# Optimization experiments

Measured on AMD Instinct MI355X. Metric: run time of the kernel, lower is better.

The kernel has to match this reference:

```python
import jax, jax.numpy as jnp
import numpy as np

WINDOW_SIZE = 11
SIGMA = 1.5
C1 = 0.01 ** 2
C2 = 0.03 ** 2


def _gaussian_window(channel, dtype):
    # 1D gaussian, normalized, then outer product -> 2D window, expanded per channel
    xs = np.arange(WINDOW_SIZE) - WINDOW_SIZE // 2
    g = np.exp(-(xs.astype(np.float64) ** 2) / (2.0 * SIGMA ** 2))
    g = (g / g.sum()).astype(np.float32)
    w2d = np.outer(g, g)  # [ws, ws]
    w = np.broadcast_to(w2d[None, None], (channel, 1, WINDOW_SIZE, WINDOW_SIZE))
    return jnp.asarray(w, dtype=dtype)


def _depthwise_conv(img, window, channel):
    pad = WINDOW_SIZE // 2
    return jax.lax.conv_general_dilated(
        img, window,
        window_strides=(1, 1),
        padding=[(pad, pad), (pad, pad)],
        dimension_numbers=('NCHW', 'OIHW', 'NCHW'),
        feature_group_count=channel)


def setup_inputs() -> dict:
    key = jax.random.key(0)
    k1, k2 = jax.random.split(key)
    shape = (16, 3, 512, 512)
    x = jax.random.uniform(k1, shape, dtype=jnp.float32)
    y = jax.random.uniform(k2, shape, dtype=jnp.float32)
    return {"x": x, "y": y}


def reference(x, y):
    channel = x.shape[-3]
    window = _gaussian_window(channel, x.dtype)

    mu1 = _depthwise_conv(x, window, channel)
    mu2 = _depthwise_conv(y, window, channel)
    mu1_sq = mu1 * mu1
    mu2_sq = mu2 * mu2
    mu1_mu2 = mu1 * mu2
    sigma1_sq = _depthwise_conv(x * x, window, channel) - mu1_sq
    sigma2_sq = _depthwise_conv(y * y, window, channel) - mu2_sq
    sigma12 = _depthwise_conv(x * y, window, channel) - mu1_mu2

    ssim_map = ((2.0 * mu1_mu2 + C1) * (2.0 * sigma12 + C2)) / (
        (mu1_sq + mu2_sq + C1) * (sigma1_sq + sigma2_sq + C2))
    # DSSIM = 1 - mean(ssim)
    return 1.0 - jnp.mean(ssim_map)
```

## Files before the change

### kernel.cpp

```cpp
#include <hip/hip_runtime.h>


typedef _Float16 half8 __attribute__((ext_vector_type(8)));
typedef _Float16 half4v __attribute__((ext_vector_type(4)));
typedef float f32x4 __attribute__((ext_vector_type(4)));
typedef float f32x8 __attribute__((ext_vector_type(8)));

#define IMG_W   512
#define IMG_H   512
#define NPLANES 48
#define BR      16
#define TP      40
#define GRX     (IMG_H / BR)
#define NBLK    (GRX * NPLANES)

__global__ __launch_bounds__(256, 3)
void dssim_main(const float* __restrict__ xin, const float* __restrict__ yin,
                float* __restrict__ partial) {
    __shared__ _Float16 ldsT[4][2][4][16][TP];
    __shared__ float wpart[4];

    const int t    = threadIdx.x;
    const int lane = t & 63;
    const int wid  = t >> 6;
    const int bn   = lane & 15;
    const int jg   = lane >> 4;
    const int r0   = blockIdx.x * BR;
    const size_t pbase = (size_t)blockIdx.y * (IMG_W * IMG_H);
    const float* __restrict__ xp = xin + pbase;
    const float* __restrict__ yp = yin + pbase;

    float ginv;
    {
        float s = 0.f;
#pragma unroll
        for (int i = 0; i < 11; ++i) {
            float d = (float)(i - 5);
            s += expf(-(d * d) * (1.0f / 4.5f));
        }
        ginv = 1.0f / s;
    }

    half8 whF, wvF;
#pragma unroll
    for (int j = 0; j < 8; ++j) {
        const int k = 8 * jg + j;
        const int dh = k - bn - 3;
        const int dv = k - bn;
        float wh = 0.f, wv = 0.f;
        if (dh >= 0 && dh < 11) {
            const float d = (float)(dh - 5);
            wh = ginv * expf(-(d * d) * (1.0f / 4.5f));
        }
        if (dv >= 0 && dv < 11) {
            const float d = (float)(dv - 5);
            wv = ginv * expf(-(d * d) * (1.0f / 4.5f));
        }
        whF[j] = (_Float16)wh;
        wvF[j] = (_Float16)wv;
    }

    const int gr0 = r0 - 5 + bn;
    const bool rowok0 = (gr0 >= 0) && (gr0 < IMG_H);
    const int gr1 = r0 + 11 + bn;
    const bool rowok1 = (bn < 10) && (gr1 < IMG_H);
    const size_t row0 = (size_t)(rowok0 ? gr0 : 0) * IMG_W;
    const size_t row1 = (size_t)(rowok1 ? gr1 : 0) * IMG_W;

    const f32x8 z8 = {0.f, 0.f, 0.f, 0.f, 0.f, 0.f, 0.f, 0.f};
    const f32x4 zf = {0.f, 0.f, 0.f, 0.f};
    const float C1 = 0.0001f, C2 = 0.0009f;
    float lsum = 0.f;

    f32x8 xs0, ys0, xs1, ys1;

#define LOADI(ii)                                                           \
    {                                                                       \
        const int col = (((wid + 4 * (ii)) << 4) + 8 * jg) - 8;             \
        const bool colok = (col >= 0) && (col < IMG_W);                     \
        const size_t co = (size_t)(colok ? col : 0);                        \
        const bool ok0 = colok && rowok0, ok1 = colok && rowok1;            \
        xs0 = ok0 ? *(const f32x8*)(xp + row0 + co) : z8;                   \
        ys0 = ok0 ? *(const f32x8*)(yp + row0 + co) : z8;                   \
        xs1 = ok1 ? *(const f32x8*)(xp + row1 + co) : z8;                   \
        ys1 = ok1 ? *(const f32x8*)(yp + row1 + co) : z8;                   \
    }

#define HCOMPI(ii)                                                          \
    {                                                                       \
        const int slot = (ii) & 1;                                          \
        _Pragma("unroll")                                                   \
        for (int rt = 0; rt < 2; ++rt) {                                    \
            const f32x8 xv = rt ? xs1 : xs0;                                \
            const f32x8 yv = rt ? ys1 : ys0;                                \
            half8 aU, aW, aU2, aW2;                                         \
            _Pragma("unroll")                                               \
            for (int d = 0; d < 8; ++d) {                                   \
                aU[d] = (_Float16)(xv[d] + yv[d]);                          \
                aW[d] = (_Float16)(xv[d] - yv[d]);                          \
            }                                                               \
            _Pragma("unroll")                                               \
            for (int d = 0; d < 8; ++d) {                                   \
                aU2[d] = aU[d] * aU[d];                                     \
                aW2[d] = aW[d] * aW[d];                                     \
            }                                                               \
            const f32x4 cU  = __builtin_amdgcn_mfma_f32_16x16x32_f16(aU,  whF, zf, 0, 0, 0); \
            const f32x4 cW  = __builtin_amdgcn_mfma_f32_16x16x32_f16(aW,  whF, zf, 0, 0, 0); \
            const f32x4 cU2 = __builtin_amdgcn_mfma_f32_16x16x32_f16(aU2, whF, zf, 0, 0, 0); \
            const f32x4 cW2 = __builtin_amdgcn_mfma_f32_16x16x32_f16(aW2, whF, zf, 0, 0, 0); \
            half4v hU, hW, hU2, hW2;                                        \
            _Pragma("unroll")                                               \
            for (int q = 0; q < 4; ++q) {                                   \
                hU[q]  = (_Float16)cU[q];                                   \
                hW[q]  = (_Float16)cW[q];                                   \
                hU2[q] = (_Float16)cU2[q];                                  \
                hW2[q] = (_Float16)cW2[q];                                  \
            }                                                               \
            const int kk = 16 * rt + 4 * jg;                                \
            *(half4v*)&ldsT[wid][slot][0][bn][kk] = hU;                     \
            *(half4v*)&ldsT[wid][slot][1][bn][kk] = hW;                     \
            *(half4v*)&ldsT[wid][slot][2][bn][kk] = hU2;                    \
            *(half4v*)&ldsT[wid][slot][3][bn][kk] = hW2;                    \
        }                                                                   \
    }

#define VBLURI(ii)                                                          \
    {                                                                       \
        const int slot = (ii) & 1;                                          \
        const half8 aTU  = *(const half8*)&ldsT[wid][slot][0][bn][8 * jg];  \
        const half8 aTW  = *(const half8*)&ldsT[wid][slot][1][bn][8 * jg];  \
        const half8 aTU2 = *(const half8*)&ldsT[wid][slot][2][bn][8 * jg];  \
        const half8 aTW2 = *(const half8*)&ldsT[wid][slot][3][bn][8 * jg];  \
        const f32x4 accU = __builtin_amdgcn_mfma_f32_16x16x32_f16(aTU,  wvF, zf, 0, 0, 0); \
        const f32x4 accW = __builtin_amdgcn_mfma_f32_16x16x32_f16(aTW,  wvF, zf, 0, 0, 0); \
        const f32x4 accP = __builtin_amdgcn_mfma_f32_16x16x32_f16(aTU2, wvF, zf, 0, 0, 0); \
        const f32x4 accQ = __builtin_amdgcn_mfma_f32_16x16x32_f16(aTW2, wvF, zf, 0, 0, 0); \
        _Pragma("unroll")                                                   \
        for (int q = 0; q < 4; ++q) {                                       \
            const float U = accU[q], W = accW[q];                           \
            const float P = accP[q], Q = accQ[q];                           \
            const float U2 = U * U, W2 = W * W;                             \
            const float A = 0.5f * (U2 + W2);                               \
            const float B = 0.5f * (U2 - W2);                               \
            const float den2 = fmaf(0.5f, P + Q, -A) + C2;                  \
            const float num2 = fmaf(0.5f, P - Q, -B) + C2;                  \
            lsum += (B + C1) * num2 * __builtin_amdgcn_rcpf((A + C1) * den2); \
        }                                                                   \
    }

    LOADI(0);
    HCOMPI(0);
#pragma unroll
    for (int i = 0; i < 8; ++i) {
        if (i + 1 < 8) LOADI(i + 1);
        VBLURI(i);
        if (i + 1 < 8) HCOMPI(i + 1);
    }

#pragma unroll
    for (int off = 32; off >= 1; off >>= 1)
        lsum += __shfl_down(lsum, off, 64);
    if (lane == 0) wpart[wid] = lsum;
    __syncthreads();
    if (t == 0) {
        partial[(size_t)blockIdx.y * GRX + blockIdx.x] =
            wpart[0] + wpart[1] + wpart[2] + wpart[3];
    }
}

__global__ __launch_bounds__(256)
void dssim_final(const float* __restrict__ partial, float* __restrict__ out) {
    __shared__ double wsum[4];
    double s = 0.0;
    for (int i = threadIdx.x; i < NBLK; i += 256) s += (double)partial[i];
#pragma unroll
    for (int off = 32; off >= 1; off >>= 1)
        s += __shfl_down(s, off, 64);
    if ((threadIdx.x & 63) == 0) wsum[threadIdx.x >> 6] = s;
    __syncthreads();
    if (threadIdx.x == 0) {
        const double tot = wsum[0] + wsum[1] + wsum[2] + wsum[3];
        out[0] = (float)(1.0 - tot / 12582912.0);
    }
}

extern "C" void kernel_launch(void* const* d_in, const int* in_sizes, int n_in,
                              void* d_out, int out_size, void* d_ws, size_t ws_size,
                              hipStream_t stream) {
    const float* x = (const float*)d_in[0];
    const float* y = (const float*)d_in[1];
    float* out = (float*)d_out;
    float* partial = (float*)d_ws;

    dim3 grid(GRX, NPLANES);
    dim3 block(256);
    dssim_main<<<grid, block, 0, stream>>>(x, y, partial);
    dssim_final<<<1, block, 0, stream>>>(partial, out);
}
```

Before: 49.01 us.

## Single-buffer LDS transpose with XOR swizzle, packed fp16 converts, higher occupancy

The per-wave LDS transpose buffer goes from double to single buffering, which halves shared memory per block. The launch bound is raised from 3 to 5 blocks per CU to use that headroom. An XOR swizzle on the column index is meant to cut LDS bank conflicts, and the scalar fp16 conversions become packed cvt_pkrtz (round toward zero) with vector half multiplies. With only one buffer there is a write-after-read hazard between iterations, unless ordering within the wave covers it. The rounding mode also changes from nearest to toward-zero.

After: 113.3 us. 2.31x slower.

```diff
diff --git a/kernel.cpp b/kernel.cpp
--- a/kernel.cpp
+++ b/kernel.cpp
@@ -3,6 +3,7 @@
 
 typedef _Float16 half8 __attribute__((ext_vector_type(8)));
 typedef _Float16 half4v __attribute__((ext_vector_type(4)));
+typedef __fp16 pk16 __attribute__((ext_vector_type(2)));
 typedef float f32x4 __attribute__((ext_vector_type(4)));
 typedef float f32x8 __attribute__((ext_vector_type(8)));
 
@@ -14,10 +15,10 @@
 #define GRX     (IMG_H / BR)
 #define NBLK    (GRX * NPLANES)
 
-__global__ __launch_bounds__(256, 3)
+__global__ __launch_bounds__(256, 5)
 void dssim_main(const float* __restrict__ xin, const float* __restrict__ yin,
                 float* __restrict__ partial) {
-    __shared__ _Float16 ldsT[4][2][4][16][TP];
+    __shared__ _Float16 ldsT[4][4][16][TP];
     __shared__ float wpart[4];
 
     const int t    = threadIdx.x;
@@ -25,6 +26,7 @@
     const int wid  = t >> 6;
     const int bn   = lane & 15;
     const int jg   = lane >> 4;
+    const int swz  = (bn & 8) << 1;
     const int r0   = blockIdx.x * BR;
     const size_t pbase = (size_t)blockIdx.y * (IMG_W * IMG_H);
     const float* __restrict__ xp = xin + pbase;
@@ -88,49 +90,53 @@
 
 #define HCOMPI(ii)                                                          \
     {                                                                       \
-        const int slot = (ii) & 1;                                          \
         _Pragma("unroll")                                                   \
         for (int rt = 0; rt < 2; ++rt) {                                    \
             const f32x8 xv = rt ? xs1 : xs0;                                \
             const f32x8 yv = rt ? ys1 : ys0;                                \
-            half8 aU, aW, aU2, aW2;                                         \
+            half8 aU, aW;                                                   \
             _Pragma("unroll")                                               \
-            for (int d = 0; d < 8; ++d) {                                   \
-                aU[d] = (_Float16)(xv[d] + yv[d]);                          \
-                aW[d] = (_Float16)(xv[d] - yv[d]);                          \
+            for (int d = 0; d < 4; ++d) {                                   \
+                const pk16 pu = __builtin_amdgcn_cvt_pkrtz(                 \
+                    xv[2 * d] + yv[2 * d], xv[2 * d + 1] + yv[2 * d + 1]);  \
+                const pk16 pw = __builtin_amdgcn_cvt_pkrtz(                 \
+                    xv[2 * d] - yv[2 * d], xv[2 * d + 1] - yv[2 * d + 1]);  \
+                aU[2 * d] = (_Float16)pu[0]; aU[2 * d + 1] = (_Float16)pu[1]; \
+                aW[2 * d] = (_Float16)pw[0]; aW[2 * d + 1] = (_Float16)pw[1]; \
             }                                                               \
-            _Pragma("unroll")                                               \
-            for (int d = 0; d < 8; ++d) {                                   \
-                aU2[d] = aU[d] * aU[d];                                     \
-                aW2[d] = aW[d] * aW[d];                                     \
-            }                                                               \
+            const half8 aU2 = aU * aU;                                      \
+            const half8 aW2 = aW * aW;                                      \
             const f32x4 cU  = __builtin_amdgcn_mfma_f32_16x16x32_f16(aU,  whF, zf, 0, 0, 0); \
             const f32x4 cW  = __builtin_amdgcn_mfma_f32_16x16x32_f16(aW,  whF, zf, 0, 0, 0); \
             const f32x4 cU2 = __builtin_amdgcn_mfma_f32_16x16x32_f16(aU2, whF, zf, 0, 0, 0); \
             const f32x4 cW2 = __builtin_amdgcn_mfma_f32_16x16x32_f16(aW2, whF, zf, 0, 0, 0); \
             half4v hU, hW, hU2, hW2;                                        \
             _Pragma("unroll")                                               \
-            for (int q = 0; q < 4; ++q) {                                   \
-                hU[q]  = (_Float16)cU[q];                                   \
-                hW[q]  = (_Float16)cW[q];                                   \
-                hU2[q] = (_Float16)cU2[q];                                  \
-                hW2[q] = (_Float16)cW2[q];                                  \
+            for (int q = 0; q < 2; ++q) {                                   \
+                const pk16 p0 = __builtin_amdgcn_cvt_pkrtz(cU[2*q],  cU[2*q+1]);  \
+                const pk16 p1 = __builtin_amdgcn_cvt_pkrtz(cW[2*q],  cW[2*q+1]);  \
+                const pk16 p2 = __builtin_amdgcn_cvt_pkrtz(cU2[2*q], cU2[2*q+1]); \
+                const pk16 p3 = __builtin_amdgcn_cvt_pkrtz(cW2[2*q], cW2[2*q+1]); \
+                hU[2*q]  = (_Float16)p0[0]; hU[2*q+1]  = (_Float16)p0[1];   \
+                hW[2*q]  = (_Float16)p1[0]; hW[2*q+1]  = (_Float16)p1[1];   \
+                hU2[2*q] = (_Float16)p2[0]; hU2[2*q+1] = (_Float16)p2[1];   \
+                hW2[2*q] = (_Float16)p3[0]; hW2[2*q+1] = (_Float16)p3[1];   \
             }                                                               \
-            const int kk = 16 * rt + 4 * jg;                                \
-            *(half4v*)&ldsT[wid][slot][0][bn][kk] = hU;                     \
-            *(half4v*)&ldsT[wid][slot][1][bn][kk] = hW;                     \
-            *(half4v*)&ldsT[wid][slot][2][bn][kk] = hU2;                    \
-            *(half4v*)&ldsT[wid][slot][3][bn][kk] = hW2;                    \
+            const int kk = (16 * rt + 4 * jg) ^ swz;                        \
+            *(half4v*)&ldsT[wid][0][bn][kk] = hU;                           \
+            *(half4v*)&ldsT[wid][1][bn][kk] = hW;                           \
+            *(half4v*)&ldsT[wid][2][bn][kk] = hU2;                          \
+            *(half4v*)&ldsT[wid][3][bn][kk] = hW2;                          \
         }                                                                   \
     }
 
 #define VBLURI(ii)                                                          \
     {                                                                       \
-        const int slot = (ii) & 1;                                          \
-        const half8 aTU  = *(const half8*)&ldsT[wid][slot][0][bn][8 * jg];  \
-        const half8 aTW  = *(const half8*)&ldsT[wid][slot][1][bn][8 * jg];  \
-        const half8 aTU2 = *(const half8*)&ldsT[wid][slot][2][bn][8 * jg];  \
-        const half8 aTW2 = *(const half8*)&ldsT[wid][slot][3][bn][8 * jg];  \
+        const int kb = (8 * jg) ^ swz;                                      \
+        const half8 aTU  = *(const half8*)&ldsT[wid][0][bn][kb];            \
+        const half8 aTW  = *(const half8*)&ldsT[wid][1][bn][kb];            \
+        const half8 aTU2 = *(const half8*)&ldsT[wid][2][bn][kb];            \
+        const half8 aTW2 = *(const half8*)&ldsT[wid][3][bn][kb];            \
         const f32x4 accU = __builtin_amdgcn_mfma_f32_16x16x32_f16(aTU,  wvF, zf, 0, 0, 0); \
         const f32x4 accW = __builtin_amdgcn_mfma_f32_16x16x32_f16(aTW,  wvF, zf, 0, 0, 0); \
         const f32x4 accP = __builtin_amdgcn_mfma_f32_16x16x32_f16(aTU2, wvF, zf, 0, 0, 0); \
```

## Keep horizontal-blur MFMA results in registers, dropping the LDS transpose

Applied to the files above, without the earlier changes.

The horizontal-pass MFMA outputs are now packed straight into register operands for the vertical pass. The operands are swapped so the output layout of the first MFMA matches the B-operand layout of the second, with the vertical weights re-indexed to suit, so the LDS store, reload and shared buffer are gone. Column bounds checks are replaced by fixed pointer offsets that clamp only the two edge lanes, and row checks now run only for edge blocks. Conversions use packed round-toward-zero f16 conversion, which changes rounding slightly and adds some risk of subtle indexing errors.

Result: slower. 53.49 us (+9.2%).

```diff
diff --git a/kernel.cpp b/kernel.cpp
--- a/kernel.cpp
+++ b/kernel.cpp
@@ -2,7 +2,7 @@
 
 
 typedef _Float16 half8 __attribute__((ext_vector_type(8)));
-typedef _Float16 half4v __attribute__((ext_vector_type(4)));
+typedef __fp16 pk16 __attribute__((ext_vector_type(2)));
 typedef float f32x4 __attribute__((ext_vector_type(4)));
 typedef float f32x8 __attribute__((ext_vector_type(8)));
 
@@ -10,14 +10,12 @@
 #define IMG_H   512
 #define NPLANES 48
 #define BR      16
-#define TP      40
 #define GRX     (IMG_H / BR)
 #define NBLK    (GRX * NPLANES)
 
 __global__ __launch_bounds__(256, 3)
 void dssim_main(const float* __restrict__ xin, const float* __restrict__ yin,
                 float* __restrict__ partial) {
-    __shared__ _Float16 ldsT[4][2][4][16][TP];
     __shared__ float wpart[4];
 
     const int t    = threadIdx.x;
@@ -26,6 +24,7 @@
     const int bn   = lane & 15;
     const int jg   = lane >> 4;
     const int r0   = blockIdx.x * BR;
+    const bool edge = (blockIdx.x == 0) || (blockIdx.x == GRX - 1);
     const size_t pbase = (size_t)blockIdx.y * (IMG_W * IMG_H);
     const float* __restrict__ xp = xin + pbase;
     const float* __restrict__ yp = yin + pbase;
@@ -46,7 +45,8 @@
     for (int j = 0; j < 8; ++j) {
         const int k = 8 * jg + j;
         const int dh = k - bn - 3;
-        const int dv = k - bn;
+        const int sigma = (j < 4) ? (4 * jg + j) : (12 + 4 * jg + j);
+        const int dv = sigma - bn;
         float wh = 0.f, wv = 0.f;
         if (dh >= 0 && dh < 11) {
             const float d = (float)(dh - 5);
@@ -67,74 +67,99 @@
     const size_t row0 = (size_t)(rowok0 ? gr0 : 0) * IMG_W;
     const size_t row1 = (size_t)(rowok1 ? gr1 : 0) * IMG_W;
 
+    const int cb = (wid << 4) + (jg << 3) - 8;
+    const float* bx0 = xp + row0 + cb;
+    const float* by0 = yp + row0 + cb;
+    const float* bx1 = xp + row1 + cb;
+    const float* by1 = yp + row1 + cb;
+
     const f32x8 z8 = {0.f, 0.f, 0.f, 0.f, 0.f, 0.f, 0.f, 0.f};
     const f32x4 zf = {0.f, 0.f, 0.f, 0.f};
     const float C1 = 0.0001f, C2 = 0.0009f;
     float lsum = 0.f;
 
     f32x8 xs0, ys0, xs1, ys1;
-
-#define LOADI(ii)                                                           \
+    half8 bU, bW, bP, bQ;
+
+#define LOADP(m)                                                            \
     {                                                                       \
-        const int col = (((wid + 4 * (ii)) << 4) + 8 * jg) - 8;             \
-        const bool colok = (col >= 0) && (col < IMG_W);                     \
-        const size_t co = (size_t)(colok ? col : 0);                        \
-        const bool ok0 = colok && rowok0, ok1 = colok && rowok1;            \
-        xs0 = ok0 ? *(const f32x8*)(xp + row0 + co) : z8;                   \
-        ys0 = ok0 ? *(const f32x8*)(yp + row0 + co) : z8;                   \
-        xs1 = ok1 ? *(const f32x8*)(xp + row1 + co) : z8;                   \
-        ys1 = ok1 ? *(const f32x8*)(yp + row1 + co) : z8;                   \
-    }
-
-#define HCOMPI(ii)                                                          \
+        int fix = 0;                                                        \
+        if ((m) == 0) fix = (wid == 0 && jg == 0) ? 8 : 0;                  \
+        if ((m) == 7) fix = (wid == 3 && jg == 3) ? -8 : 0;                 \
+        const int off = 64 * (m);                                           \
+        xs0 = *(const f32x8*)(bx0 + off + fix);                             \
+        ys0 = *(const f32x8*)(by0 + off + fix);                             \
+        xs1 = *(const f32x8*)(bx1 + off + fix);                             \
+        ys1 = *(const f32x8*)(by1 + off + fix);                             \
+        if ((m) == 0) {                                                     \
+            if (wid == 0 && jg == 0) { xs0 = z8; ys0 = z8; xs1 = z8; ys1 = z8; } \
+        }                                                                   \
+        if ((m) == 7) {                                                     \
+            if (wid == 3 && jg == 3) { xs0 = z8; ys0 = z8; xs1 = z8; ys1 = z8; } \
+        }                                                                   \
+        if (edge) {                                                         \
+            if (!rowok0) { xs0 = z8; ys0 = z8; }                            \
+            if (!rowok1) { xs1 = z8; ys1 = z8; }                            \
+        }                                                                   \
+    }
+
+#define HCOMP()                                                             \
     {                                                                       \
-        const int slot = (ii) & 1;                                          \
+        half8 aU0, aW0, aU1, aW1;                                           \
         _Pragma("unroll")                                                   \
-        for (int rt = 0; rt < 2; ++rt) {                                    \
-            const f32x8 xv = rt ? xs1 : xs0;                                \
-            const f32x8 yv = rt ? ys1 : ys0;                                \
-            half8 aU, aW, aU2, aW2;                                         \
-            _Pragma("unroll")                                               \
-            for (int d = 0; d < 8; ++d) {                                   \
-                aU[d] = (_Float16)(xv[d] + yv[d]);                          \
-                aW[d] = (_Float16)(xv[d] - yv[d]);                          \
-            }                                                               \
-            _Pragma("unroll")                                               \
-            for (int d = 0; d < 8; ++d) {                                   \
-                aU2[d] = aU[d] * aU[d];                                     \
-                aW2[d] = aW[d] * aW[d];                                     \
-            }                                                               \
-            const f32x4 cU  = __builtin_amdgcn_mfma_f32_16x16x32_f16(aU,  whF, zf, 0, 0, 0); \
-            const f32x4 cW  = __builtin_amdgcn_mfma_f32_16x16x32_f16(aW,  whF, zf, 0, 0, 0); \
-            const f32x4 cU2 = __builtin_amdgcn_mfma_f32_16x16x32_f16(aU2, whF, zf, 0, 0, 0); \
-            const f32x4 cW2 = __builtin_amdgcn_mfma_f32_16x16x32_f16(aW2, whF, zf, 0, 0, 0); \
-            half4v hU, hW, hU2, hW2;                                        \
-            _Pragma("unroll")                                               \
-            for (int q = 0; q < 4; ++q) {                                   \
-                hU[q]  = (_Float16)cU[q];                                   \
-                hW[q]  = (_Float16)cW[q];                                   \
-                hU2[q] = (_Float16)cU2[q];                                  \
-                hW2[q] = (_Float16)cW2[q];                                  \
-            }                                                               \
-            const int kk = 16 * rt + 4 * jg;                                \
-            *(half4v*)&ldsT[wid][slot][0][bn][kk] = hU;                     \
-            *(half4v*)&ldsT[wid][slot][1][bn][kk] = hW;                     \
-            *(half4v*)&ldsT[wid][slot][2][bn][kk] = hU2;                    \
-            *(half4v*)&ldsT[wid][slot][3][bn][kk] = hW2;                    \
-        }                                                                   \
-    }
-
-#define VBLURI(ii)                                                          \
+        for (int d = 0; d < 4; ++d) {                                       \
+            const pk16 pu0 = __builtin_amdgcn_cvt_pkrtz(                    \
+                xs0[2 * d] + ys0[2 * d], xs0[2 * d + 1] + ys0[2 * d + 1]);  \
+            const pk16 pw0 = __builtin_amdgcn_cvt_pkrtz(                    \
+                xs0[2 * d] - ys0[2 * d], xs0[2 * d + 1] - ys0[2 * d + 1]);  \
+            const pk16 pu1 = __builtin_amdgcn_cvt_pkrtz(                    \
+                xs1[2 * d] + ys1[2 * d], xs1[2 * d + 1] + ys1[2 * d + 1]);  \
+            const pk16 pw1 = __builtin_amdgcn_cvt_pkrtz(                    \
+                xs1[2 * d] - ys1[2 * d], xs1[2 * d + 1] - ys1[2 * d + 1]);  \
+            aU0[2 * d] = (_Float16)pu0[0]; aU0[2 * d + 1] = (_Float16)pu0[1]; \
+            aW0[2 * d] = (_Float16)pw0[0]; aW0[2 * d + 1] = (_Float16)pw0[1]; \
+            aU1[2 * d] = (_Float16)pu1[0]; aU1[2 * d + 1] = (_Float16)pu1[1]; \
+            aW1[2 * d] = (_Float16)pw1[0]; aW1[2 * d + 1] = (_Float16)pw1[1]; \
+        }                                                                   \
+        const half8 aP0 = aU0 * aU0;                                        \
+        const half8 aQ0 = aW0 * aW0;                                        \
+        const half8 aP1 = aU1 * aU1;                                        \
+        const half8 aQ1 = aW1 * aW1;                                        \
+        const f32x4 cU0 = __builtin_amdgcn_mfma_f32_16x16x32_f16(aU0, whF, zf, 0, 0, 0); \
+        const f32x4 cW0 = __builtin_amdgcn_mfma_f32_16x16x32_f16(aW0, whF, zf, 0, 0, 0); \
+        const f32x4 cP0 = __builtin_amdgcn_mfma_f32_16x16x32_f16(aP0, whF, zf, 0, 0, 0); \
+        const f32x4 cQ0 = __builtin_amdgcn_mfma_f32_16x16x32_f16(aQ0, whF, zf, 0, 0, 0); \
+        const f32x4 cU1 = __builtin_amdgcn_mfma_f32_16x16x32_f16(aU1, whF, zf, 0, 0, 0); \
+        const f32x4 cW1 = __builtin_amdgcn_mfma_f32_16x16x32_f16(aW1, whF, zf, 0, 0, 0); \
+        const f32x4 cP1 = __builtin_amdgcn_mfma_f32_16x16x32_f16(aP1, whF, zf, 0, 0, 0); \
+        const f32x4 cQ1 = __builtin_amdgcn_mfma_f32_16x16x32_f16(aQ1, whF, zf, 0, 0, 0); \
+        _Pragma("unroll")                                                   \
+        for (int q = 0; q < 2; ++q) {                                       \
+            const pk16 u0 = __builtin_amdgcn_cvt_pkrtz(cU0[2*q], cU0[2*q+1]); \
+            const pk16 w0 = __builtin_amdgcn_cvt_pkrtz(cW0[2*q], cW0[2*q+1]); \
+            const pk16 p0 = __builtin_amdgcn_cvt_pkrtz(cP0[2*q], cP0[2*q+1]); \
+            const pk16 q0 = __builtin_amdgcn_cvt_pkrtz(cQ0[2*q], cQ0[2*q+1]); \
+            const pk16 u1 = __builtin_amdgcn_cvt_pkrtz(cU1[2*q], cU1[2*q+1]); \
+            const pk16 w1 = __builtin_amdgcn_cvt_pkrtz(cW1[2*q], cW1[2*q+1]); \
+            const pk16 p1 = __builtin_amdgcn_cvt_pkrtz(cP1[2*q], cP1[2*q+1]); \
+            const pk16 q1 = __builtin_amdgcn_cvt_pkrtz(cQ1[2*q], cQ1[2*q+1]); \
+            bU[2*q]     = (_Float16)u0[0]; bU[2*q + 1]     = (_Float16)u0[1]; \
+            bW[2*q]     = (_Float16)w0[0]; bW[2*q + 1]     = (_Float16)w0[1]; \
+            bP[2*q]     = (_Float16)p0[0]; bP[2*q + 1]     = (_Float16)p0[1]; \
+            bQ[2*q]     = (_Float16)q0[0]; bQ[2*q + 1]     = (_Float16)q0[1]; \
+            bU[2*q + 4] = (_Float16)u1[0]; bU[2*q + 5]     = (_Float16)u1[1]; \
+            bW[2*q + 4] = (_Float16)w1[0]; bW[2*q + 5]     = (_Float16)w1[1]; \
+            bP[2*q + 4] = (_Float16)p1[0]; bP[2*q + 5]     = (_Float16)p1[1]; \
+            bQ[2*q + 4] = (_Float16)q1[0]; bQ[2*q + 5]     = (_Float16)q1[1]; \
+        }                                                                   \
+    }
+
+#define VBLUR()                                                             \
     {                                                                       \
-        const int slot = (ii) & 1;                                          \
-        const half8 aTU  = *(const half8*)&ldsT[wid][slot][0][bn][8 * jg];  \
-        const half8 aTW  = *(const half8*)&ldsT[wid][slot][1][bn][8 * jg];  \
-        const half8 aTU2 = *(const half8*)&ldsT[wid][slot][2][bn][8 * jg];  \
-        const half8 aTW2 = *(const half8*)&ldsT[wid][slot][3][bn][8 * jg];  \
-        const f32x4 accU = __builtin_amdgcn_mfma_f32_16x16x32_f16(aTU,  wvF, zf, 0, 0, 0); \
-        const f32x4 accW = __builtin_amdgcn_mfma_f32_16x16x32_f16(aTW,  wvF, zf, 0, 0, 0); \
-        const f32x4 accP = __builtin_amdgcn_mfma_f32_16x16x32_f16(aTU2, wvF, zf, 0, 0, 0); \
-        const f32x4 accQ = __builtin_amdgcn_mfma_f32_16x16x32_f16(aTW2, wvF, zf, 0, 0, 0); \
+        const f32x4 accU = __builtin_amdgcn_mfma_f32_16x16x32_f16(wvF, bU, zf, 0, 0, 0); \
+        const f32x4 accW = __builtin_amdgcn_mfma_f32_16x16x32_f16(wvF, bW, zf, 0, 0, 0); \
+        const f32x4 accP = __builtin_amdgcn_mfma_f32_16x16x32_f16(wvF, bP, zf, 0, 0, 0); \
+        const f32x4 accQ = __builtin_amdgcn_mfma_f32_16x16x32_f16(wvF, bQ, zf, 0, 0, 0); \
         _Pragma("unroll")                                                   \
         for (int q = 0; q < 4; ++q) {                                       \
             const float U = accU[q], W = accW[q];                           \
@@ -148,13 +173,13 @@
         }                                                                   \
     }
 
-    LOADI(0);
-    HCOMPI(0);
+    LOADP(0);
+    HCOMP();
 #pragma unroll
     for (int i = 0; i < 8; ++i) {
-        if (i + 1 < 8) LOADI(i + 1);
-        VBLURI(i);
-        if (i + 1 < 8) HCOMPI(i + 1);
+        if (i < 7) LOADP(i + 1);
+        VBLUR();
+        if (i < 7) HCOMP();
     }
 
 #pragma unroll
```
